# Optimization experiments

Hardware: AMD Instinct MI355X
Metric: run time of the kernel (lower is better)

The kernel has to match this reference:

```python
import jax, jax.numpy as jnp
import numpy as np

B, C, H, W = 4, 512, 32, 32
NH = 8
HD = C // NH
PH, PW = 2, 4
NPR = PH * PW
HIDDEN = int(C * 2.0)
EPS = 1e-5

def _bn(x, p):
    g, b, m, v = p[0], p[1], p[2], p[3]
    s = g * jax.lax.rsqrt(v + EPS)
    return x * s[None, :, None, None] + (b - m * s)[None, :, None, None]

def _ln(x, p):
    mu = x.mean(-1, keepdims=True)
    var = ((x - mu) ** 2).mean(-1, keepdims=True)
    return (x - mu) * jax.lax.rsqrt(var + EPS) * p[0] + p[1]

def _dwconv(x, w):
    return jax.lax.conv_general_dilated(
        x, w, (1, 1), 'SAME',
        dimension_numbers=('NCHW', 'OIHW', 'NCHW'),
        feature_group_count=x.shape[1])

def _pw(x, w):
    # 1x1 conv, no bias: w is (O, I, 1, 1)
    return jnp.einsum('bchw,oc->bohw', x, w[:, :, 0, 0])

def _pool(x, ph, pw):
    # adaptive avg pool when output evenly divides input
    b, c, h, w = x.shape
    return x.reshape(b, c, ph, h // ph, pw, w // pw).mean(axis=(3, 5))

def _gelu(x):
    return jax.nn.gelu(x, approximate=False)

def _coords(h, w):
    y = jnp.linspace(0.0, 1.0, h)
    x = jnp.linspace(0.0, 1.0, w)
    gy, gx = jnp.meshgrid(y, x, indexing='ij')
    return jnp.stack([gy, gx], axis=-1).reshape(-1, 2)


def setup_inputs() -> dict:
    key = jax.random.key(0)
    ks = iter(jax.random.split(key, 64))
    def nrm(shape, s=0.02):
        return jax.random.normal(next(ks), shape, jnp.float32) * s
    def bnp():
        return jnp.stack([1.0 + nrm((C,), 0.1), nrm((C,), 0.1),
                          nrm((C,), 0.1), 1.0 + jnp.abs(nrm((C,), 0.2))])
    def lnp(c=C):
        return jnp.stack([jnp.ones((c,), jnp.float32), jnp.zeros((c,), jnp.float32)])
    return {
        'fused': jax.random.normal(next(ks), (B, C, H, W), jnp.float32),
        'depth': jax.random.normal(next(ks), (B, C, H, W), jnp.float32),
        'pg_dw_w': nrm((C, 1, 3, 3)), 'pg_bn1': bnp(),
        'pg_pw_w': nrm((C, C, 1, 1)), 'pg_bn2': bnp(),
        'prompt_embed': nrm((1, NPR, C)), 'pg_ln': lnp(),
        'gp_dw_w': nrm((C, 1, 3, 3)), 'gp_bn': bnp(),
        'gp_pw_w': nrm((1, C, 1, 1)), 'gp_pw_b': jnp.zeros((1,), jnp.float32),
        'gp_weight': jnp.ones((2, 1, 1, 1), jnp.float32),
        'ln1': lnp(),
        'wq': nrm((C, C)), 'wk': nrm((C, C)), 'wv': nrm((C, C)), 'wo': nrm((C, C)),
        'ln2': lnp(),
        'mlp_w1': nrm((HIDDEN, C)), 'mlp_b1': jnp.zeros((HIDDEN,), jnp.float32),
        'mlp_w2': nrm((C, HIDDEN)), 'mlp_b2': jnp.zeros((C,), jnp.float32),
        'op_dw_w': nrm((C, 1, 3, 3)), 'op_bn1': bnp(),
        'op_pw_w': nrm((C, C, 1, 1)), 'op_bn2': bnp(),
    }


def reference(fused, depth, pg_dw_w, pg_bn1, pg_pw_w, pg_bn2, prompt_embed, pg_ln,
              gp_dw_w, gp_bn, gp_pw_w, gp_pw_b, gp_weight,
              ln1, wq, wk, wv, wo, ln2, mlp_w1, mlp_b1, mlp_w2, mlp_b2,
              op_dw_w, op_bn1, op_pw_w, op_bn2):
    b = fused.shape[0]
    # --- DepthPromptGenerator ---
    pp = _gelu(_bn(_dwconv(depth, pg_dw_w), pg_bn1))
    pp = _gelu(_bn(_pw(pp, pg_pw_w), pg_bn2))
    prompt = _pool(pp, PH, PW).reshape(b, C, NPR).transpose(0, 2, 1)  # (B, P, C)
    prompt = _ln(prompt + prompt_embed, pg_ln)
    # --- GeometryPriorGenerator ---
    ds = _gelu(_bn(_dwconv(depth, gp_dw_w), gp_bn))
    ds = _pw(ds, gp_pw_w) + gp_pw_b[None, :, None, None]  # (B,1,H,W)
    img_d = ds.reshape(b, H * W)
    pr_d = _pool(ds, PH, PW).reshape(b, NPR)
    jd = jnp.concatenate([pr_d, img_d], axis=1)  # (B, N) depth scalar per token
    coords = jnp.concatenate([_coords(PH, PW), _coords(H, W)], axis=0)  # (N,2)
    pos = jnp.abs(coords[:, None, :] - coords[None, :, :]).sum(-1)  # (N,N) L1 distance
    decay = jnp.log(1.0 - 2.0 ** (-1.0 - 4.0 * jnp.arange(NH, dtype=jnp.float32) / NH))
    pos_mask = pos[None, :, :] * decay[:, None, None]  # (NH,N,N)
    depth_mask = jnp.abs(jd[:, :, None] - jd[:, None, :])[:, None, :, :] * decay[None, :, None, None]
    bias = gp_weight[0, 0, 0, 0] * pos_mask[None] + gp_weight[1, 0, 0, 0] * depth_mask  # (B,NH,N,N)
    # --- GeometryAwarePromptMixer ---
    img_tok = fused.reshape(b, C, H * W).transpose(0, 2, 1)  # (B,HW,C)
    jt = jnp.concatenate([prompt, img_tok], axis=1)  # (B,N,C)
    n = jt.shape[1]
    x = _ln(jt, ln1)
    q = jnp.einsum('bnc,dc->bnd', x, wq).reshape(b, n, NH, HD).transpose(0, 2, 1, 3)
    k = jnp.einsum('bnc,dc->bnd', x, wk).reshape(b, n, NH, HD).transpose(0, 2, 1, 3)
    v = jnp.einsum('bnc,dc->bnd', x, wv).reshape(b, n, NH, HD).transpose(0, 2, 1, 3)
    logits = jnp.einsum('bhnd,bhmd->bhnm', q, k) * (HD ** -0.5) + bias
    attn = jax.nn.softmax(logits, axis=-1)
    ao = jnp.einsum('bhnm,bhmd->bhnd', attn, v).transpose(0, 2, 1, 3).reshape(b, n, C)
    jt = jt + jnp.einsum('bnc,dc->bnd', ao, wo)
    h = _gelu(jnp.einsum('bnc,hc->bnh', _ln(jt, ln2), mlp_w1) + mlp_b1)
    jt = jt + jnp.einsum('bnh,ch->bnc', h, mlp_w2) + mlp_b2
    enh = jt[:, NPR:, :].transpose(0, 2, 1).reshape(b, C, H, W)
    # --- out_proj ---
    o = _gelu(_bn(_dwconv(enh, op_dw_w), op_bn1))
    o = _bn(_pw(o, op_pw_w), op_bn2)
    return fused + o
```

## Files before the change

kernel.cpp:

```cpp
#include <hip/hip_runtime.h>
#include <math.h>

typedef __attribute__((ext_vector_type(8))) short bf16x8;
typedef __attribute__((ext_vector_type(4))) float f32x4;

#define CH 512
#define HWP 1024
#define NTOK 1032
#define NTP 1088
#define NPRM 8
#define BB 4
#define EPSV 1e-5f
#define MTOK 4128
#define MPAD 4224

__device__ __forceinline__ float gelu_f(float x) {
  return 0.5f * x * (1.0f + erff(x * 0.70710678118654752440f));
}

__device__ __forceinline__ ushort f2bf(float x) {
  union { float f; unsigned u; } v; v.f = x;
  unsigned r = v.u + 0x7FFF + ((v.u >> 16) & 1);
  return (ushort)(r >> 16);
}

__device__ __forceinline__ float bf2f(ushort u) {
  union { unsigned u; float f; } v; v.u = ((unsigned)u) << 16;
  return v.f;
}

__device__ __forceinline__ void gl16(const ushort* g, ushort* s) {
  __builtin_amdgcn_global_load_lds(
      (const __attribute__((address_space(1))) unsigned int*)g,
      (__attribute__((address_space(3))) unsigned int*)s,
      16, 0, 0);
}

__global__ __launch_bounds__(256) void convw(
    const float* __restrict__ wq, const float* __restrict__ wk, const float* __restrict__ wv,
    const float* __restrict__ wo, const float* __restrict__ w1, const float* __restrict__ w2,
    const float* __restrict__ pgw, const float* __restrict__ opw, const float* __restrict__ gpw,
    ushort* __restrict__ out)
{
  const int total = 2621952;
  for (int i = blockIdx.x * 256 + threadIdx.x; i < total; i += gridDim.x * 256) {
    const float* src; int off;
    if (i < 262144)       { src = wq;  off = i; }
    else if (i < 524288)  { src = wk;  off = i - 262144; }
    else if (i < 786432)  { src = wv;  off = i - 524288; }
    else if (i < 1048576) { src = wo;  off = i - 786432; }
    else if (i < 1572864) { src = w1;  off = i - 1048576; }
    else if (i < 2097152) { src = w2;  off = i - 1572864; }
    else if (i < 2359296) { src = pgw; off = i - 2097152; }
    else if (i < 2621440) { src = opw; off = i - 2359296; }
    else                  { src = gpw; off = i - 2621440; }
    out[i] = f2bf(src[off]);
  }
}

__global__ __launch_bounds__(256) void dwt_fused(
    const float* __restrict__ in, const float* __restrict__ w9p,
    const float* __restrict__ bn, ushort* __restrict__ outT)
{
  __shared__ float tile[32][33];
  const int y = blockIdx.x;
  const int c0 = blockIdx.y * 32;
  const int b = blockIdx.z;
  const int tx = threadIdx.x, ty = threadIdx.y;
  #pragma unroll
  for (int i = 0; i < 4; ++i) {
    int c = c0 + ty + i * 8;
    const float* ip = in + ((size_t)(b * CH + c)) * HWP;
    const float* wp = w9p + c * 9;
    float acc = 0.0f;
    #pragma unroll
    for (int dy = 0; dy < 3; ++dy) {
      int yy = y + dy - 1;
      if ((unsigned)yy < 32u) {
        #pragma unroll
        for (int dx = 0; dx < 3; ++dx) {
          int xx = tx + dx - 1;
          if ((unsigned)xx < 32u) acc += ip[yy * 32 + xx] * wp[dy * 3 + dx];
        }
      }
    }
    float g = bn[c], be = bn[CH + c], mm = bn[2 * CH + c], vv = bn[3 * CH + c];
    float s = g * rsqrtf(vv + EPSV);
    tile[ty + i * 8][tx] = gelu_f(acc * s + (be - mm * s));
  }
  __syncthreads();
  #pragma unroll
  for (int i = 0; i < 4; ++i)
    outT[((size_t)(b * HWP + y * 32 + ty + i * 8)) * CH + c0 + tx] = f2bf(tile[tx][ty + i * 8]);
}

__device__ __forceinline__ void stage2(const ushort* ga, const ushort* gb,
                                       ushort* la, ushort* lb, int w)
{
  gl16(ga + w * 8,       la + w * 512);
  gl16(ga + (w + 4) * 8, la + (w + 4) * 512);
  gl16(gb + w * 8,       lb + w * 512);
  gl16(gb + (w + 4) * 8, lb + (w + 4) * 512);
}

__device__ __forceinline__ void comp64(const ushort* la, const ushort* lb,
                                       int wr, int wc, int l, f32x4 (&acc)[2][2])
{
  bf16x8 af[2][2], bfv[2][2];
  #pragma unroll
  for (int ks = 0; ks < 2; ++ks) {
    int kb = ks * 4 + (l >> 4);
    #pragma unroll
    for (int mf = 0; mf < 2; ++mf)
      af[mf][ks] = *(const bf16x8*)(la + (kb * 64 + wr + mf * 16 + (l & 15)) * 8);
    #pragma unroll
    for (int nf = 0; nf < 2; ++nf)
      bfv[nf][ks] = *(const bf16x8*)(lb + (kb * 64 + wc + nf * 16 + (l & 15)) * 8);
  }
  #pragma unroll
  for (int mf = 0; mf < 2; ++mf) {
    #pragma unroll
    for (int nf = 0; nf < 2; ++nf) {
      acc[mf][nf] = __builtin_amdgcn_mfma_f32_16x16x32_bf16(af[mf][0], bfv[nf][0], acc[mf][nf], 0, 0, 0);
      acc[mf][nf] = __builtin_amdgcn_mfma_f32_16x16x32_bf16(af[mf][1], bfv[nf][1], acc[mf][nf], 0, 0, 0);
    }
  }
}

#define G64_PRE(Arow, Brow, Kdim) \
  __shared__ ushort sA[8192], sB[8192]; \
  f32x4 acc[2][2]; \
  { f32x4 z = {0.f, 0.f, 0.f, 0.f}; acc[0][0] = z; acc[0][1] = z; acc[1][0] = z; acc[1][1] = z; } \
  const int l = threadIdx.x & 63, w = threadIdx.x >> 6; \
  const int wr = (w >> 1) * 32, wc = (w & 1) * 32; \
  stage2(Arow, Brow, sA, sB, w); \
  __syncthreads(); \
  const int nk = (Kdim) / 64; \
  for (int kt = 0; kt < nk; ++kt) { \
    if (kt + 1 < nk) \
      stage2(Arow + (kt + 1) * 64, Brow + (kt + 1) * 64, \
             sA + ((kt + 1) & 1) * 4096, sB + ((kt + 1) & 1) * 4096, w); \
    comp64(sA + (kt & 1) * 4096, sB + (kt & 1) * 4096, wr, wc, l, acc); \
    __syncthreads(); \
  }

__global__ __launch_bounds__(256) void gemm_qkv64(
    const ushort* __restrict__ A, const ushort* __restrict__ B,
    ushort* __restrict__ qh, ushort* __restrict__ kh, ushort* __restrict__ vt)
{
  const int n0 = blockIdx.x * 64, m0 = blockIdx.y * 64;
  const ushort* Arow = A + ((size_t)m0 + (threadIdx.x & 63)) * 512;
  const ushort* Brow = B + ((size_t)n0 + (threadIdx.x & 63)) * 512;
  G64_PRE(Arow, Brow, 512)
  #pragma unroll
  for (int nf = 0; nf < 2; ++nf) {
    int n = n0 + wc + nf * 16 + (l & 15);
    #pragma unroll
    for (int mf = 0; mf < 2; ++mf) {
      #pragma unroll
      for (int r = 0; r < 4; ++r) {
        int m = m0 + wr + mf * 16 + (l >> 4) * 4 + r;
        if (m < MTOK) {
          int b = m / NTOK;
          int tok = m - b * NTOK;
          float val = acc[mf][nf][r];
          if (n < 512) {
            qh[((size_t)((b * 8 + (n >> 6)) * NTP) + tok) * 64 + (n & 63)] = f2bf(val);
          } else if (n < 1024) {
            int n2 = n - 512;
            kh[((size_t)((b * 8 + (n2 >> 6)) * NTP) + tok) * 64 + (n2 & 63)] = f2bf(val);
          } else {
            int n2 = n - 1024;
            vt[((size_t)((b * 8 + (n2 >> 6)) * 64) + (n2 & 63)) * NTP + tok] = f2bf(val);
          }
        }
      }
    }
  }
}

__global__ __launch_bounds__(256) void gemm_res64(
    const ushort* __restrict__ A, const ushort* __restrict__ B,
    float* __restrict__ Cf, const float* __restrict__ bias, int Kdim)
{
  const int n0 = blockIdx.x * 64, m0 = blockIdx.y * 64;
  const ushort* Arow = A + ((size_t)m0 + (threadIdx.x & 63)) * Kdim;
  const ushort* Brow = B + ((size_t)n0 + (threadIdx.x & 63)) * Kdim;
  G64_PRE(Arow, Brow, Kdim)
  #pragma unroll
  for (int nf = 0; nf < 2; ++nf) {
    int n = n0 + wc + nf * 16 + (l & 15);
    float bv = bias ? bias[n] : 0.0f;
    #pragma unroll
    for (int mf = 0; mf < 2; ++mf) {
      #pragma unroll
      for (int r = 0; r < 4; ++r) {
        int m = m0 + wr + mf * 16 + (l >> 4) * 4 + r;
        if (m < MTOK) Cf[(size_t)m * 512 + n] += acc[mf][nf][r] + bv;
      }
    }
  }
}

__global__ __launch_bounds__(256) void gemm_gelu64(
    const ushort* __restrict__ A, const ushort* __restrict__ B,
    const float* __restrict__ bias, ushort* __restrict__ Ob)
{
  const int n0 = blockIdx.x * 64, m0 = blockIdx.y * 64;
  const ushort* Arow = A + ((size_t)m0 + (threadIdx.x & 63)) * 512;
  const ushort* Brow = B + ((size_t)n0 + (threadIdx.x & 63)) * 512;
  G64_PRE(Arow, Brow, 512)
  #pragma unroll
  for (int nf = 0; nf < 2; ++nf) {
    int n = n0 + wc + nf * 16 + (l & 15);
    float bv = bias[n];
    #pragma unroll
    for (int mf = 0; mf < 2; ++mf) {
      #pragma unroll
      for (int r = 0; r < 4; ++r) {
        int m = m0 + wr + mf * 16 + (l >> 4) * 4 + r;
        if (m < MTOK) Ob[(size_t)m * 1024 + n] = f2bf(gelu_f(acc[mf][nf][r] + bv));
      }
    }
  }
}

template<int MODE>
__global__ __launch_bounds__(256) void gemm_pw64(
    const ushort* __restrict__ A, const ushort* __restrict__ B,
    const float* __restrict__ bnp, const float* __restrict__ res, float* __restrict__ Of)
{
  const int hw0 = blockIdx.x * 64, m0 = blockIdx.y * 64;
  const int b = blockIdx.z;
  const ushort* Arow = A + ((size_t)m0 + (threadIdx.x & 63)) * 512;
  const ushort* Brow = B + ((size_t)(b * HWP + hw0) + (threadIdx.x & 63)) * 512;
  G64_PRE(Arow, Brow, 512)
  #pragma unroll
  for (int mf = 0; mf < 2; ++mf) {
    #pragma unroll
    for (int r = 0; r < 4; ++r) {
      int o = m0 + wr + mf * 16 + (l >> 4) * 4 + r;
      float g = bnp[o], be = bnp[CH + o], mm = bnp[2 * CH + o], vv = bnp[3 * CH + o];
      float s = g * rsqrtf(vv + EPSV);
      float sh = be - mm * s;
      #pragma unroll
      for (int nf = 0; nf < 2; ++nf) {
        int hw = hw0 + wc + nf * 16 + (l & 15);
        float x = acc[mf][nf][r] * s + sh;
        size_t oi = ((size_t)(b * CH + o)) * HWP + hw;
        if (MODE == 0) Of[oi] = gelu_f(x);
        else Of[oi] = x + res[oi];
      }
    }
  }
}

__global__ __launch_bounds__(128) void pp_pool(const float* __restrict__ pp, float* __restrict__ ppool)
{
  int bc = blockIdx.x;
  int b = bc >> 9, c = bc & 511;
  __shared__ float sums[8];
  if (threadIdx.x < 8) sums[threadIdx.x] = 0.0f;
  __syncthreads();
  const float* ip = pp + (size_t)bc * HWP;
  float s0 = 0.0f, s1 = 0.0f;
  #pragma unroll
  for (int kq = 0; kq < 8; ++kq) {
    float val = ip[threadIdx.x + kq * 128];
    if (kq < 4) s0 += val; else s1 += val;
  }
  int pxr = (threadIdx.x & 31) >> 3;
  atomicAdd(&sums[pxr], s0);
  atomicAdd(&sums[4 + pxr], s1);
  __syncthreads();
  if (threadIdx.x < 8)
    ppool[((size_t)b * 8 + threadIdx.x) * CH + c] = sums[threadIdx.x] * (1.0f / 128.0f);
}

__global__ __launch_bounds__(128) void prompt_ln(
    const float* __restrict__ ppool, const float* __restrict__ embed,
    const float* __restrict__ lnp, float* __restrict__ jt)
{
  int rB = blockIdx.x;
  int b = rB >> 3, pI = rB & 7;
  float4 val = ((const float4*)(ppool + (size_t)rB * CH))[threadIdx.x];
  float4 e = ((const float4*)(embed + (size_t)pI * CH))[threadIdx.x];
  val.x += e.x; val.y += e.y; val.z += e.z; val.w += e.w;
  float sum = val.x + val.y + val.z + val.w;
  float sq = val.x * val.x + val.y * val.y + val.z * val.z + val.w * val.w;
  #pragma unroll
  for (int off = 1; off < 64; off <<= 1) { sum += __shfl_xor(sum, off); sq += __shfl_xor(sq, off); }
  __shared__ float s2[4];
  if ((threadIdx.x & 63) == 0) { s2[(threadIdx.x >> 6) * 2] = sum; s2[(threadIdx.x >> 6) * 2 + 1] = sq; }
  __syncthreads();
  sum = s2[0] + s2[2]; sq = s2[1] + s2[3];
  float mu = sum * (1.0f / 512.0f);
  float var = sq * (1.0f / 512.0f) - mu * mu;
  float rstd = rsqrtf(var + EPSV);
  int c = threadIdx.x * 4;
  float4 o;
  o.x = (val.x - mu) * rstd * lnp[c] + lnp[CH + c];
  o.y = (val.y - mu) * rstd * lnp[c + 1] + lnp[CH + c + 1];
  o.z = (val.z - mu) * rstd * lnp[c + 2] + lnp[CH + c + 2];
  o.w = (val.w - mu) * rstd * lnp[c + 3] + lnp[CH + c + 3];
  ((float4*)(jt + ((size_t)(b * NTOK + pI)) * CH))[threadIdx.x] = o;
}

__global__ __launch_bounds__(256) void gp_dot(
    const ushort* __restrict__ xT, const ushort* __restrict__ wbf,
    const float* __restrict__ b0, float* __restrict__ jdv)
{
  const int b = blockIdx.y;
  const int row0 = blockIdx.x * 16;
  const int l = threadIdx.x & 63, w = threadIdx.x >> 6;
  bf16x8 wv = *(const bf16x8*)(wbf + l * 8);
  float wf[8];
  #pragma unroll
  for (int j = 0; j < 8; ++j) wf[j] = bf2f((ushort)wv[j]);
  #pragma unroll
  for (int rr = 0; rr < 4; ++rr) {
    int hw = row0 + w * 4 + rr;
    bf16x8 xv = *(const bf16x8*)(xT + ((size_t)(b * HWP + hw)) * CH + l * 8);
    float s = 0.0f;
    #pragma unroll
    for (int j = 0; j < 8; ++j) s += wf[j] * bf2f((ushort)xv[j]);
    #pragma unroll
    for (int off = 1; off < 64; off <<= 1) s += __shfl_xor(s, off);
    if (l == 0) jdv[b * NTP + NPRM + hw] = s + b0[0];
  }
}

__global__ __launch_bounds__(256) void jd_pool(float* jd)
{
  int b = blockIdx.x;
  __shared__ float sums[8];
  if (threadIdx.x < 8) sums[threadIdx.x] = 0.0f;
  __syncthreads();
  #pragma unroll
  for (int kq = 0; kq < 4; ++kq) {
    int px = threadIdx.x + kq * 256;
    int y = px >> 5, x = px & 31;
    int r = (y >> 4) * 4 + (x >> 3);
    atomicAdd(&sums[r], jd[b * NTP + NPRM + px]);
  }
  __syncthreads();
  if (threadIdx.x < 8) jd[b * NTP + threadIdx.x] = sums[threadIdx.x] * (1.0f / 128.0f);
}

__global__ __launch_bounds__(256) void img_to_tokens(const float* __restrict__ fused, float* __restrict__ jt)
{
  __shared__ float tile[32][33];
  int hw0 = blockIdx.x * 32, c0 = blockIdx.y * 32, b = blockIdx.z;
  int tx = threadIdx.x, ty = threadIdx.y;
  #pragma unroll
  for (int i = 0; i < 4; ++i)
    tile[ty + i * 8][tx] = fused[((size_t)(b * CH + c0 + ty + i * 8)) * HWP + hw0 + tx];
  __syncthreads();
  #pragma unroll
  for (int i = 0; i < 4; ++i)
    jt[((size_t)(b * NTOK + NPRM + hw0 + ty + i * 8)) * CH + c0 + tx] = tile[tx][ty + i * 8];
}

__global__ __launch_bounds__(256) void tokens_to_img(const float* __restrict__ jt, float* __restrict__ out)
{
  __shared__ float tile[32][33];
  int hw0 = blockIdx.x * 32, c0 = blockIdx.y * 32, b = blockIdx.z;
  int tx = threadIdx.x, ty = threadIdx.y;
  #pragma unroll
  for (int i = 0; i < 4; ++i)
    tile[ty + i * 8][tx] = jt[((size_t)(b * NTOK + NPRM + hw0 + ty + i * 8)) * CH + c0 + tx];
  __syncthreads();
  #pragma unroll
  for (int i = 0; i < 4; ++i)
    out[((size_t)(b * CH + c0 + ty + i * 8)) * HWP + hw0 + tx] = tile[tx][ty + i * 8];
}

__global__ __launch_bounds__(128) void ln_rows_bf(
    const float* __restrict__ in, const float* __restrict__ lnp, ushort* __restrict__ out)
{
  int row = blockIdx.x;
  float4 val = ((const float4*)(in + (size_t)row * CH))[threadIdx.x];
  float sum = val.x + val.y + val.z + val.w;
  float sq = val.x * val.x + val.y * val.y + val.z * val.z + val.w * val.w;
  #pragma unroll
  for (int off = 1; off < 64; off <<= 1) { sum += __shfl_xor(sum, off); sq += __shfl_xor(sq, off); }
  __shared__ float s2[4];
  if ((threadIdx.x & 63) == 0) { s2[(threadIdx.x >> 6) * 2] = sum; s2[(threadIdx.x >> 6) * 2 + 1] = sq; }
  __syncthreads();
  sum = s2[0] + s2[2]; sq = s2[1] + s2[3];
  float mu = sum * (1.0f / 512.0f);
  float var = sq * (1.0f / 512.0f) - mu * mu;
  float rstd = rsqrtf(var + EPSV);
  int c = threadIdx.x * 4;
  ushort4 o;
  o.x = f2bf((val.x - mu) * rstd * lnp[c] + lnp[CH + c]);
  o.y = f2bf((val.y - mu) * rstd * lnp[c + 1] + lnp[CH + c + 1]);
  o.z = f2bf((val.z - mu) * rstd * lnp[c + 2] + lnp[CH + c + 2]);
  o.w = f2bf((val.w - mu) * rstd * lnp[c + 3] + lnp[CH + c + 3]);
  *(ushort4*)(out + (size_t)row * CH + c) = o;
}

__device__ __forceinline__ void tok_coord(int idx, float& y, float& x)
{
  if (idx < NPRM) { y = (float)(idx >> 2); x = (float)(idx & 3) * (1.0f / 3.0f); }
  else { int t = idx - NPRM; y = (float)(t >> 5) * (1.0f / 31.0f); x = (float)(t & 31) * (1.0f / 31.0f); }
}

__global__ __launch_bounds__(256) void attn_mfma2(
    const ushort* __restrict__ qh, const ushort* __restrict__ kh,
    const ushort* __restrict__ vT, const float* __restrict__ jd,
    const float* __restrict__ gw, ushort* __restrict__ ao)
{
  __shared__ ushort sK[8192], sV[8192];
  __shared__ ushort Pl[4][16][72];
  const int t = threadIdx.x, l = t & 63, w = t >> 6;
  const int h = blockIdx.y, b = blockIdx.z;
  const int i0 = blockIdx.x * 64 + w * 16;
  const ushort* Q = qh + (size_t)(b * 8 + h) * NTP * 64;
  const ushort* K = kh + (size_t)(b * 8 + h) * NTP * 64;
  const ushort* V = vT + (size_t)(b * 8 + h) * 64 * NTP;
  const float decay = logf(1.0f - exp2f(-1.0f - 0.5f * (float)h));
  const float g0 = gw[0] * decay, g1 = gw[1] * decay;

  bf16x8 qf0 = *(const bf16x8*)(Q + (size_t)(i0 + (l & 15)) * 64 + (l >> 4) * 8);
  bf16x8 qf1 = *(const bf16x8*)(Q + (size_t)(i0 + (l & 15)) * 64 + 32 + (l >> 4) * 8);

  float yi[4], xi[4], jdi[4];
  #pragma unroll
  for (int r = 0; r < 4; ++r) {
    int i = i0 + (l >> 4) * 4 + r;
    tok_coord(i, yi[r], xi[r]);
    jdi[r] = jd[b * NTP + i];
  }

  float m_r[4] = { -1e30f, -1e30f, -1e30f, -1e30f };
  float l_r[4] = { 0.f, 0.f, 0.f, 0.f };
  f32x4 of[4];
  { f32x4 z = {0.f, 0.f, 0.f, 0.f};
    #pragma unroll
    for (int d = 0; d < 4; ++d) of[d] = z; }

#define ASTAGE(buf, j0s) { \
    const ushort* gk = K + (size_t)((j0s) + l) * 64; \
    const ushort* gv = V + (size_t)l * NTP + (j0s); \
    gl16(gk + w * 8,       sK + (buf) * 4096 + w * 512); \
    gl16(gk + (w + 4) * 8, sK + (buf) * 4096 + (w + 4) * 512); \
    gl16(gv + w * 8,       sV + (buf) * 4096 + w * 512); \
    gl16(gv + (w + 4) * 8, sV + (buf) * 4096 + (w + 4) * 512); }

  ASTAGE(0, 0)
  __syncthreads();
  const int NJT = 17;
  for (int jti = 0; jti < NJT; ++jti) {
    const int j0 = jti * 64;
    if (jti + 1 < NJT) ASTAGE((jti + 1) & 1, j0 + 64)
    const ushort* bK = sK + (jti & 1) * 4096;
    const ushort* bV = sV + (jti & 1) * 4096;

    f32x4 sfr[4];
    #pragma unroll
    for (int jf = 0; jf < 4; ++jf) {
      bf16x8 k0 = *(const bf16x8*)(bK + (((l >> 4)) * 64 + jf * 16 + (l & 15)) * 8);
      bf16x8 k1 = *(const bf16x8*)(bK + ((4 + (l >> 4)) * 64 + jf * 16 + (l & 15)) * 8);
      f32x4 z = {0.f, 0.f, 0.f, 0.f};
      z = __builtin_amdgcn_mfma_f32_16x16x32_bf16(qf0, k0, z, 0, 0, 0);
      z = __builtin_amdgcn_mfma_f32_16x16x32_bf16(qf1, k1, z, 0, 0, 0);
      sfr[jf] = z;
    }
    float pvv[4][4];
    float mt[4] = { -1e30f, -1e30f, -1e30f, -1e30f };
    #pragma unroll
    for (int jf = 0; jf < 4; ++jf) {
      int jj = j0 + jf * 16 + (l & 15);
      float yj, xj;
      tok_coord(jj, yj, xj);
      float jdj = jd[b * NTP + jj];
      bool valid = jj < NTOK;
      #pragma unroll
      for (int r = 0; r < 4; ++r) {
        float bias = g0 * (fabsf(yi[r] - yj) + fabsf(xi[r] - xj)) + g1 * fabsf(jdi[r] - jdj);
        float sv = valid ? (sfr[jf][r] * 0.125f + bias) : -1e30f;
        pvv[jf][r] = sv;
        mt[r] = fmaxf(mt[r], sv);
      }
    }
    #pragma unroll
    for (int r = 0; r < 4; ++r) {
      #pragma unroll
      for (int off = 1; off < 16; off <<= 1) mt[r] = fmaxf(mt[r], __shfl_xor(mt[r], off));
    }
    float alpha[4], ls[4];
    #pragma unroll
    for (int r = 0; r < 4; ++r) {
      float mn = fmaxf(m_r[r], mt[r]);
      alpha[r] = __expf(m_r[r] - mn);
      m_r[r] = mn;
      ls[r] = 0.f;
    }
    #pragma unroll
    for (int jf = 0; jf < 4; ++jf) {
      #pragma unroll
      for (int r = 0; r < 4; ++r) {
        float pp = __expf(pvv[jf][r] - m_r[r]);
        pvv[jf][r] = pp;
        ls[r] += pp;
      }
    }
    #pragma unroll
    for (int r = 0; r < 4; ++r) {
      #pragma unroll
      for (int off = 1; off < 16; off <<= 1) ls[r] += __shfl_xor(ls[r], off);
      l_r[r] = l_r[r] * alpha[r] + ls[r];
    }
    #pragma unroll
    for (int d = 0; d < 4; ++d) {
      #pragma unroll
      for (int r = 0; r < 4; ++r) of[d][r] *= alpha[r];
    }
    #pragma unroll
    for (int jf = 0; jf < 4; ++jf) {
      #pragma unroll
      for (int r = 0; r < 4; ++r)
        Pl[w][(l >> 4) * 4 + r][jf * 16 + (l & 15)] = f2bf(pvv[jf][r]);
    }
    asm volatile("s_waitcnt lgkmcnt(0)" ::: "memory");
    bf16x8 pa0 = *(const bf16x8*)&Pl[w][l & 15][(l >> 4) * 8];
    bf16x8 pa1 = *(const bf16x8*)&Pl[w][l & 15][32 + (l >> 4) * 8];
    #pragma unroll
    for (int df = 0; df < 4; ++df) {
      bf16x8 v0 = *(const bf16x8*)(bV + (((l >> 4)) * 64 + df * 16 + (l & 15)) * 8);
      bf16x8 v1 = *(const bf16x8*)(bV + ((4 + (l >> 4)) * 64 + df * 16 + (l & 15)) * 8);
      of[df] = __builtin_amdgcn_mfma_f32_16x16x32_bf16(pa0, v0, of[df], 0, 0, 0);
      of[df] = __builtin_amdgcn_mfma_f32_16x16x32_bf16(pa1, v1, of[df], 0, 0, 0);
    }
    __syncthreads();
  }
  #pragma unroll
  for (int r = 0; r < 4; ++r) {
    int i = i0 + (l >> 4) * 4 + r;
    if (i < NTOK) {
      float inv = 1.0f / l_r[r];
      #pragma unroll
      for (int df = 0; df < 4; ++df)
        ao[((size_t)(b * NTOK + i)) * 512 + h * 64 + df * 16 + (l & 15)] = f2bf(of[df][r] * inv);
    }
  }
}

extern "C" void kernel_launch(void* const* d_in, const int* in_sizes, int n_in,
                              void* d_out, int out_size, void* d_ws, size_t ws_size,
                              hipStream_t stream)
{
  const float* fused = (const float*)d_in[0];
  const float* depth = (const float*)d_in[1];
  const float* pg_dw_w = (const float*)d_in[2];
  const float* pg_bn1 = (const float*)d_in[3];
  const float* pg_pw_w = (const float*)d_in[4];
  const float* pg_bn2 = (const float*)d_in[5];
  const float* prompt_embed = (const float*)d_in[6];
  const float* pg_ln = (const float*)d_in[7];
  const float* gp_dw_w = (const float*)d_in[8];
  const float* gp_bn = (const float*)d_in[9];
  const float* gp_pw_w = (const float*)d_in[10];
  const float* gp_pw_b = (const float*)d_in[11];
  const float* gp_weight = (const float*)d_in[12];
  const float* ln1 = (const float*)d_in[13];
  const float* wq = (const float*)d_in[14];
  const float* wk = (const float*)d_in[15];
  const float* wv = (const float*)d_in[16];
  const float* wo = (const float*)d_in[17];
  const float* ln2 = (const float*)d_in[18];
  const float* mlp_w1 = (const float*)d_in[19];
  const float* mlp_b1 = (const float*)d_in[20];
  const float* mlp_w2 = (const float*)d_in[21];
  const float* mlp_b2 = (const float*)d_in[22];
  const float* op_dw_w = (const float*)d_in[23];
  const float* op_bn1 = (const float*)d_in[24];
  const float* op_pw_w = (const float*)d_in[25];
  const float* op_bn2 = (const float*)d_in[26];
  float* out = (float*)d_out;

  char* p = (char*)d_ws;
  auto alloc = [&](size_t bytes) { char* r = p; p += (bytes + 1023) & ~(size_t)1023; return r; };
  float*  jt    = (float*) alloc((size_t)MTOK * 512 * 4);
  ushort* xb    = (ushort*)alloc((size_t)MPAD * 512 * 2);
  ushort* hb    = (ushort*)alloc((size_t)MPAD * 1024 * 2);
  ushort* ao    = (ushort*)alloc((size_t)MPAD * 512 * 2);
  ushort* qhB   = (ushort*)alloc((size_t)32 * NTP * 64 * 2);
  ushort* khB   = (ushort*)alloc((size_t)32 * NTP * 64 * 2);
  ushort* vTB   = (ushort*)alloc((size_t)32 * NTP * 64 * 2);
  ushort* dwT1  = (ushort*)alloc((size_t)BB * HWP * CH * 2);
  ushort* dwT2  = (ushort*)alloc((size_t)BB * HWP * CH * 2);
  float*  ppf   = (float*) alloc((size_t)BB * CH * HWP * 4);
  float*  Bf    = (float*) alloc((size_t)BB * CH * HWP * 4);
  float*  jdv   = (float*) alloc((size_t)BB * NTP * 4);
  float*  ppool = (float*) alloc((size_t)BB * 8 * CH * 4);
  ushort* wbf   = (ushort*)alloc((size_t)2621952 * 2);

  ushort* wqkv_bf = wbf;
  ushort* wo_bf   = wbf + 786432;
  ushort* w1_bf   = wbf + 1048576;
  ushort* w2_bf   = wbf + 1572864;
  ushort* pgw_bf  = wbf + 2097152;
  ushort* opw_bf  = wbf + 2359296;
  ushort* gpw_bf  = wbf + 2621440;

  hipLaunchKernelGGL(convw, dim3(4096), dim3(256), 0, stream,
                     wq, wk, wv, wo, mlp_w1, mlp_w2, pg_pw_w, op_pw_w, gp_pw_w, wbf);

  hipLaunchKernelGGL(dwt_fused, dim3(32, 16, BB), dim3(32, 8), 0, stream, depth, pg_dw_w, pg_bn1, dwT1);
  hipLaunchKernelGGL(gemm_pw64<0>, dim3(16, 8, BB), dim3(256), 0, stream, pgw_bf, dwT1, pg_bn2, (const float*)nullptr, ppf);
  hipLaunchKernelGGL(pp_pool, dim3(BB * CH), dim3(128), 0, stream, ppf, ppool);
  hipLaunchKernelGGL(prompt_ln, dim3(BB * NPRM), dim3(128), 0, stream, ppool, prompt_embed, pg_ln, jt);

  hipLaunchKernelGGL(dwt_fused, dim3(32, 16, BB), dim3(32, 8), 0, stream, depth, gp_dw_w, gp_bn, dwT2);
  hipLaunchKernelGGL(gp_dot, dim3(64, BB), dim3(256), 0, stream, dwT2, gpw_bf, gp_pw_b, jdv);
  hipLaunchKernelGGL(jd_pool, dim3(BB), dim3(256), 0, stream, jdv);

  hipLaunchKernelGGL(img_to_tokens, dim3(32, 16, BB), dim3(32, 8), 0, stream, fused, jt);
  hipLaunchKernelGGL(ln_rows_bf, dim3(MTOK), dim3(128), 0, stream, jt, ln1, xb);
  hipLaunchKernelGGL(gemm_qkv64, dim3(24, 65), dim3(256), 0, stream, xb, wqkv_bf, qhB, khB, vTB);
  hipLaunchKernelGGL(attn_mfma2, dim3(17, 8, BB), dim3(256), 0, stream, qhB, khB, vTB, jdv, gp_weight, ao);
  hipLaunchKernelGGL(gemm_res64, dim3(8, 65), dim3(256), 0, stream, ao, wo_bf, jt, (const float*)nullptr, 512);
  hipLaunchKernelGGL(ln_rows_bf, dim3(MTOK), dim3(128), 0, stream, jt, ln2, xb);
  hipLaunchKernelGGL(gemm_gelu64, dim3(16, 65), dim3(256), 0, stream, xb, w1_bf, mlp_b1, hb);
  hipLaunchKernelGGL(gemm_res64, dim3(8, 65), dim3(256), 0, stream, hb, w2_bf, jt, mlp_b2, 1024);

  hipLaunchKernelGGL(tokens_to_img, dim3(32, 16, BB), dim3(32, 8), 0, stream, jt, Bf);
  hipLaunchKernelGGL(dwt_fused, dim3(32, 16, BB), dim3(32, 8), 0, stream, Bf, op_dw_w, op_bn1, dwT1);
  hipLaunchKernelGGL(gemm_pw64<1>, dim3(16, 8, BB), dim3(256), 0, stream, opw_bf, dwT1, op_bn2, fused, out);
}
```

Baseline: 389.2 us.

## Enlarge GEMM tiles to 128x128 with swizzled LDS and fold softmax scale into Q

Replaces the 64x64 MFMA GEMM core with a 128x128 tile in which each wave computes a 64x64 sub-tile. LDS staging now uses an XOR swizzle to avoid bank conflicts and a row-major 64-wide K layout. All GEMM launches shrink their grids to match. The attention softmax scale and log2e are folded into Q at QKV write-out and into the bias decay, so the inner loop can use exp2f without a per-element multiply. Larger tiles raise data reuse and MFMA density but give fewer blocks, roughly 132–528 per GEMM, which may underfill the 256 CUs, and they use more registers and LDS.

```diff
diff --git a/kernel.cpp b/kernel.cpp
--- a/kernel.cpp
+++ b/kernel.cpp
@@ -13,6 +13,8 @@
 #define EPSV 1e-5f
 #define MTOK 4128
 #define MPAD 4224
+#define QSCL 0.18033688f
+#define LOG2E 1.44269504f
 
 __device__ __forceinline__ float gelu_f(float x) {
   return 0.5f * x * (1.0f + erff(x * 0.70710678118654752440f));
@@ -94,78 +96,79 @@
     outT[((size_t)(b * HWP + y * 32 + ty + i * 8)) * CH + c0 + tx] = f2bf(tile[tx][ty + i * 8]);
 }
 
-__device__ __forceinline__ void stage2(const ushort* ga, const ushort* gb,
-                                       ushort* la, ushort* lb, int w)
-{
-  gl16(ga + w * 8,       la + w * 512);
-  gl16(ga + (w + 4) * 8, la + (w + 4) * 512);
-  gl16(gb + w * 8,       lb + w * 512);
-  gl16(gb + (w + 4) * 8, lb + (w + 4) * 512);
-}
-
-__device__ __forceinline__ void comp64(const ushort* la, const ushort* lb,
-                                       int wr, int wc, int l, f32x4 (&acc)[2][2])
-{
-  bf16x8 af[2][2], bfv[2][2];
+__device__ __forceinline__ void stage128(const ushort* pA, const ushort* pB,
+                                         ushort* lA, ushort* lB,
+                                         int w, int KA, int KB)
+{
+  #pragma unroll
+  for (int j = 0; j < 4; ++j) {
+    gl16(pA + (size_t)j * 8 * KA, lA + (w * 32 + j * 8) * 64);
+    gl16(pB + (size_t)j * 8 * KB, lB + (w * 32 + j * 8) * 64);
+  }
+}
+
+__device__ __forceinline__ void comp128(const ushort* lA, const ushort* lB,
+                                        int wm, int wn, int l, f32x4 (&acc)[4][4])
+{
   #pragma unroll
   for (int ks = 0; ks < 2; ++ks) {
     int kb = ks * 4 + (l >> 4);
-    #pragma unroll
-    for (int mf = 0; mf < 2; ++mf)
-      af[mf][ks] = *(const bf16x8*)(la + (kb * 64 + wr + mf * 16 + (l & 15)) * 8);
-    #pragma unroll
-    for (int nf = 0; nf < 2; ++nf)
-      bfv[nf][ks] = *(const bf16x8*)(lb + (kb * 64 + wc + nf * 16 + (l & 15)) * 8);
-  }
-  #pragma unroll
-  for (int mf = 0; mf < 2; ++mf) {
-    #pragma unroll
-    for (int nf = 0; nf < 2; ++nf) {
-      acc[mf][nf] = __builtin_amdgcn_mfma_f32_16x16x32_bf16(af[mf][0], bfv[nf][0], acc[mf][nf], 0, 0, 0);
-      acc[mf][nf] = __builtin_amdgcn_mfma_f32_16x16x32_bf16(af[mf][1], bfv[nf][1], acc[mf][nf], 0, 0, 0);
-    }
-  }
-}
-
-#define G64_PRE(Arow, Brow, Kdim) \
-  __shared__ ushort sA[8192], sB[8192]; \
-  f32x4 acc[2][2]; \
-  { f32x4 z = {0.f, 0.f, 0.f, 0.f}; acc[0][0] = z; acc[0][1] = z; acc[1][0] = z; acc[1][1] = z; } \
+    int swz = ((kb ^ (l & 7)) * 8);
+    bf16x8 af[4], bfv[4];
+    #pragma unroll
+    for (int mf = 0; mf < 4; ++mf)
+      af[mf] = *(const bf16x8*)(lA + (wm + mf * 16 + (l & 15)) * 64 + swz);
+    #pragma unroll
+    for (int nf = 0; nf < 4; ++nf)
+      bfv[nf] = *(const bf16x8*)(lB + (wn + nf * 16 + (l & 15)) * 64 + swz);
+    #pragma unroll
+    for (int mf = 0; mf < 4; ++mf) {
+      #pragma unroll
+      for (int nf = 0; nf < 4; ++nf)
+        acc[mf][nf] = __builtin_amdgcn_mfma_f32_16x16x32_bf16(af[mf], bfv[nf], acc[mf][nf], 0, 0, 0);
+    }
+  }
+}
+
+#define G128_PRE(Abase, Bbase, KA, KB, Kdim) \
+  __shared__ ushort sA[2][8192], sB[2][8192]; \
+  f32x4 acc[4][4]; \
+  { f32x4 z = {0.f, 0.f, 0.f, 0.f}; \
+    _Pragma("unroll") for (int i = 0; i < 4; ++i) { _Pragma("unroll") for (int j = 0; j < 4; ++j) acc[i][j] = z; } } \
   const int l = threadIdx.x & 63, w = threadIdx.x >> 6; \
-  const int wr = (w >> 1) * 32, wc = (w & 1) * 32; \
-  stage2(Arow, Brow, sA, sB, w); \
+  const int wm = (w >> 1) * 64, wn = (w & 1) * 64; \
+  const ushort* pA = (Abase) + (size_t)(w * 32 + (l >> 3)) * (KA) + ((l & 7) ^ (l >> 3)) * 8; \
+  const ushort* pB = (Bbase) + (size_t)(w * 32 + (l >> 3)) * (KB) + ((l & 7) ^ (l >> 3)) * 8; \
+  stage128(pA, pB, sA[0], sB[0], w, KA, KB); \
   __syncthreads(); \
   const int nk = (Kdim) / 64; \
   for (int kt = 0; kt < nk; ++kt) { \
     if (kt + 1 < nk) \
-      stage2(Arow + (kt + 1) * 64, Brow + (kt + 1) * 64, \
-             sA + ((kt + 1) & 1) * 4096, sB + ((kt + 1) & 1) * 4096, w); \
-    comp64(sA + (kt & 1) * 4096, sB + (kt & 1) * 4096, wr, wc, l, acc); \
+      stage128(pA + (kt + 1) * 64, pB + (kt + 1) * 64, sA[(kt + 1) & 1], sB[(kt + 1) & 1], w, KA, KB); \
+    comp128(sA[kt & 1], sB[kt & 1], wm, wn, l, acc); \
     __syncthreads(); \
   }
 
-__global__ __launch_bounds__(256) void gemm_qkv64(
+__global__ __launch_bounds__(256) void gemm_qkv128(
     const ushort* __restrict__ A, const ushort* __restrict__ B,
     ushort* __restrict__ qh, ushort* __restrict__ kh, ushort* __restrict__ vt)
 {
-  const int n0 = blockIdx.x * 64, m0 = blockIdx.y * 64;
-  const ushort* Arow = A + ((size_t)m0 + (threadIdx.x & 63)) * 512;
-  const ushort* Brow = B + ((size_t)n0 + (threadIdx.x & 63)) * 512;
-  G64_PRE(Arow, Brow, 512)
-  #pragma unroll
-  for (int nf = 0; nf < 2; ++nf) {
-    int n = n0 + wc + nf * 16 + (l & 15);
-    #pragma unroll
-    for (int mf = 0; mf < 2; ++mf) {
+  const int n0 = blockIdx.x * 128, m0 = blockIdx.y * 128;
+  G128_PRE(A + (size_t)m0 * 512, B + (size_t)n0 * 512, 512, 512, 512)
+  #pragma unroll
+  for (int nf = 0; nf < 4; ++nf) {
+    int n = n0 + wn + nf * 16 + (l & 15);
+    #pragma unroll
+    for (int mf = 0; mf < 4; ++mf) {
       #pragma unroll
       for (int r = 0; r < 4; ++r) {
-        int m = m0 + wr + mf * 16 + (l >> 4) * 4 + r;
+        int m = m0 + wm + mf * 16 + (l >> 4) * 4 + r;
         if (m < MTOK) {
           int b = m / NTOK;
           int tok = m - b * NTOK;
           float val = acc[mf][nf][r];
           if (n < 512) {
-            qh[((size_t)((b * 8 + (n >> 6)) * NTP) + tok) * 64 + (n & 63)] = f2bf(val);
+            qh[((size_t)((b * 8 + (n >> 6)) * NTP) + tok) * 64 + (n & 63)] = f2bf(val * QSCL);
           } else if (n < 1024) {
             int n2 = n - 512;
             kh[((size_t)((b * 8 + (n2 >> 6)) * NTP) + tok) * 64 + (n2 & 63)] = f2bf(val);
@@ -179,46 +182,42 @@
   }
 }
 
-__global__ __launch_bounds__(256) void gemm_res64(
+__global__ __launch_bounds__(256) void gemm_res128(
     const ushort* __restrict__ A, const ushort* __restrict__ B,
     float* __restrict__ Cf, const float* __restrict__ bias, int Kdim)
 {
-  const int n0 = blockIdx.x * 64, m0 = blockIdx.y * 64;
-  const ushort* Arow = A + ((size_t)m0 + (threadIdx.x & 63)) * Kdim;
-  const ushort* Brow = B + ((size_t)n0 + (threadIdx.x & 63)) * Kdim;
-  G64_PRE(Arow, Brow, Kdim)
-  #pragma unroll
-  for (int nf = 0; nf < 2; ++nf) {
-    int n = n0 + wc + nf * 16 + (l & 15);
+  const int n0 = blockIdx.x * 128, m0 = blockIdx.y * 128;
+  G128_PRE(A + (size_t)m0 * Kdim, B + (size_t)n0 * Kdim, Kdim, Kdim, Kdim)
+  #pragma unroll
+  for (int nf = 0; nf < 4; ++nf) {
+    int n = n0 + wn + nf * 16 + (l & 15);
     float bv = bias ? bias[n] : 0.0f;
     #pragma unroll
-    for (int mf = 0; mf < 2; ++mf) {
+    for (int mf = 0; mf < 4; ++mf) {
       #pragma unroll
       for (int r = 0; r < 4; ++r) {
-        int m = m0 + wr + mf * 16 + (l >> 4) * 4 + r;
+        int m = m0 + wm + mf * 16 + (l >> 4) * 4 + r;
         if (m < MTOK) Cf[(size_t)m * 512 + n] += acc[mf][nf][r] + bv;
       }
     }
   }
 }
 
-__global__ __launch_bounds__(256) void gemm_gelu64(
+__global__ __launch_bounds__(256) void gemm_gelu128(
     const ushort* __restrict__ A, const ushort* __restrict__ B,
     const float* __restrict__ bias, ushort* __restrict__ Ob)
 {
-  const int n0 = blockIdx.x * 64, m0 = blockIdx.y * 64;
-  const ushort* Arow = A + ((size_t)m0 + (threadIdx.x & 63)) * 512;
-  const ushort* Brow = B + ((size_t)n0 + (threadIdx.x & 63)) * 512;
-  G64_PRE(Arow, Brow, 512)
-  #pragma unroll
-  for (int nf = 0; nf < 2; ++nf) {
-    int n = n0 + wc + nf * 16 + (l & 15);
+  const int n0 = blockIdx.x * 128, m0 = blockIdx.y * 128;
+  G128_PRE(A + (size_t)m0 * 512, B + (size_t)n0 * 512, 512, 512, 512)
+  #pragma unroll
+  for (int nf = 0; nf < 4; ++nf) {
+    int n = n0 + wn + nf * 16 + (l & 15);
     float bv = bias[n];
     #pragma unroll
-    for (int mf = 0; mf < 2; ++mf) {
+    for (int mf = 0; mf < 4; ++mf) {
       #pragma unroll
       for (int r = 0; r < 4; ++r) {
-        int m = m0 + wr + mf * 16 + (l >> 4) * 4 + r;
+        int m = m0 + wm + mf * 16 + (l >> 4) * 4 + r;
         if (m < MTOK) Ob[(size_t)m * 1024 + n] = f2bf(gelu_f(acc[mf][nf][r] + bv));
       }
     }
@@ -226,26 +225,24 @@
 }
 
 template<int MODE>
-__global__ __launch_bounds__(256) void gemm_pw64(
+__global__ __launch_bounds__(256) void gemm_pw128(
     const ushort* __restrict__ A, const ushort* __restrict__ B,
     const float* __restrict__ bnp, const float* __restrict__ res, float* __restrict__ Of)
 {
-  const int hw0 = blockIdx.x * 64, m0 = blockIdx.y * 64;
+  const int hw0 = blockIdx.x * 128, m0 = blockIdx.y * 128;
   const int b = blockIdx.z;
-  const ushort* Arow = A + ((size_t)m0 + (threadIdx.x & 63)) * 512;
-  const ushort* Brow = B + ((size_t)(b * HWP + hw0) + (threadIdx.x & 63)) * 512;
-  G64_PRE(Arow, Brow, 512)
-  #pragma unroll
-  for (int mf = 0; mf < 2; ++mf) {
+  G128_PRE(A + (size_t)m0 * 512, B + (size_t)(b * HWP + hw0) * 512, 512, 512, 512)
+  #pragma unroll
+  for (int mf = 0; mf < 4; ++mf) {
     #pragma unroll
     for (int r = 0; r < 4; ++r) {
-      int o = m0 + wr + mf * 16 + (l >> 4) * 4 + r;
+      int o = m0 + wm + mf * 16 + (l >> 4) * 4 + r;
       float g = bnp[o], be = bnp[CH + o], mm = bnp[2 * CH + o], vv = bnp[3 * CH + o];
       float s = g * rsqrtf(vv + EPSV);
       float sh = be - mm * s;
       #pragma unroll
-      for (int nf = 0; nf < 2; ++nf) {
-        int hw = hw0 + wc + nf * 16 + (l & 15);
+      for (int nf = 0; nf < 4; ++nf) {
+        int hw = hw0 + wn + nf * 16 + (l & 15);
         float x = acc[mf][nf][r] * s + sh;
         size_t oi = ((size_t)(b * CH + o)) * HWP + hw;
         if (MODE == 0) Of[oi] = gelu_f(x);
@@ -419,7 +416,7 @@
   const ushort* Q = qh + (size_t)(b * 8 + h) * NTP * 64;
   const ushort* K = kh + (size_t)(b * 8 + h) * NTP * 64;
   const ushort* V = vT + (size_t)(b * 8 + h) * 64 * NTP;
-  const float decay = logf(1.0f - exp2f(-1.0f - 0.5f * (float)h));
+  const float decay = logf(1.0f - exp2f(-1.0f - 0.5f * (float)h)) * LOG2E;
   const float g0 = gw[0] * decay, g1 = gw[1] * decay;
 
   bf16x8 qf0 = *(const bf16x8*)(Q + (size_t)(i0 + (l & 15)) * 64 + (l >> 4) * 8);
@@ -479,7 +476,7 @@
       #pragma unroll
       for (int r = 0; r < 4; ++r) {
         float bias = g0 * (fabsf(yi[r] - yj) + fabsf(xi[r] - xj)) + g1 * fabsf(jdi[r] - jdj);
-        float sv = valid ? (sfr[jf][r] * 0.125f + bias) : -1e30f;
+        float sv = valid ? (sfr[jf][r] + bias) : -1e30f;
         pvv[jf][r] = sv;
         mt[r] = fmaxf(mt[r], sv);
       }
@@ -493,7 +490,7 @@
     #pragma unroll
     for (int r = 0; r < 4; ++r) {
       float mn = fmaxf(m_r[r], mt[r]);
-      alpha[r] = __expf(m_r[r] - mn);
+      alpha[r] = exp2f(m_r[r] - mn);
       m_r[r] = mn;
       ls[r] = 0.f;
     }
@@ -501,7 +498,7 @@
     for (int jf = 0; jf < 4; ++jf) {
       #pragma unroll
       for (int r = 0; r < 4; ++r) {
-        float pp = __expf(pvv[jf][r] - m_r[r]);
+        float pp = exp2f(pvv[jf][r] - m_r[r]);
         pvv[jf][r] = pp;
         ls[r] += pp;
       }
@@ -609,7 +606,7 @@
                      wq, wk, wv, wo, mlp_w1, mlp_w2, pg_pw_w, op_pw_w, gp_pw_w, wbf);
 
   hipLaunchKernelGGL(dwt_fused, dim3(32, 16, BB), dim3(32, 8), 0, stream, depth, pg_dw_w, pg_bn1, dwT1);
-  hipLaunchKernelGGL(gemm_pw64<0>, dim3(16, 8, BB), dim3(256), 0, stream, pgw_bf, dwT1, pg_bn2, (const float*)nullptr, ppf);
+  hipLaunchKernelGGL(gemm_pw128<0>, dim3(8, 4, BB), dim3(256), 0, stream, pgw_bf, dwT1, pg_bn2, (const float*)nullptr, ppf);
   hipLaunchKernelGGL(pp_pool, dim3(BB * CH), dim3(128), 0, stream, ppf, ppool);
   hipLaunchKernelGGL(prompt_ln, dim3(BB * NPRM), dim3(128), 0, stream, ppool, prompt_embed, pg_ln, jt);
 
@@ -619,14 +616,14 @@
 
   hipLaunchKernelGGL(img_to_tokens, dim3(32, 16, BB), dim3(32, 8), 0, stream, fused, jt);
   hipLaunchKernelGGL(ln_rows_bf, dim3(MTOK), dim3(128), 0, stream, jt, ln1, xb);
-  hipLaunchKernelGGL(gemm_qkv64, dim3(24, 65), dim3(256), 0, stream, xb, wqkv_bf, qhB, khB, vTB);
+  hipLaunchKernelGGL(gemm_qkv128, dim3(12, 33), dim3(256), 0, stream, xb, wqkv_bf, qhB, khB, vTB);
   hipLaunchKernelGGL(attn_mfma2, dim3(17, 8, BB), dim3(256), 0, stream, qhB, khB, vTB, jdv, gp_weight, ao);
-  hipLaunchKernelGGL(gemm_res64, dim3(8, 65), dim3(256), 0, stream, ao, wo_bf, jt, (const float*)nullptr, 512);
+  hipLaunchKernelGGL(gemm_res128, dim3(4, 33), dim3(256), 0, stream, ao, wo_bf, jt, (const float*)nullptr, 512);
   hipLaunchKernelGGL(ln_rows_bf, dim3(MTOK), dim3(128), 0, stream, jt, ln2, xb);
-  hipLaunchKernelGGL(gemm_gelu64, dim3(16, 65), dim3(256), 0, stream, xb, w1_bf, mlp_b1, hb);
-  hipLaunchKernelGGL(gemm_res64, dim3(8, 65), dim3(256), 0, stream, hb, w2_bf, jt, mlp_b2, 1024);
+  hipLaunchKernelGGL(gemm_gelu128, dim3(8, 33), dim3(256), 0, stream, xb, w1_bf, mlp_b1, hb);
+  hipLaunchKernelGGL(gemm_res128, dim3(4, 33), dim3(256), 0, stream, hb, w2_bf, jt, mlp_b2, 1024);
 
   hipLaunchKernelGGL(tokens_to_img, dim3(32, 16, BB), dim3(32, 8), 0, stream, jt, Bf);
   hipLaunchKernelGGL(dwt_fused, dim3(32, 16, BB), dim3(32, 8), 0, stream, Bf, op_dw_w, op_bn1, dwT1);
-  hipLaunchKernelGGL(gemm_pw64<1>, dim3(16, 8, BB), dim3(256), 0, stream, opw_bf, dwT1, op_bn2, fused, out);
-}
+  hipLaunchKernelGGL(gemm_pw128<1>, dim3(8, 4, BB), dim3(256), 0, stream, opw_bf, dwT1, op_bn2, fused, out);
+}
```

Result: no change. 390.3 us (+0.3%).
